# Kernel optimization log

Measured on AMD Instinct MI355X. Metric: run time of the kernel, lower is better.

Reference implementation:

```python
import jax, jax.numpy as jnp
import numpy as np

T, B, H, E, V = 128, 64, 512, 256, 32000
UNK = 2
EPS = 1e-10


def setup_inputs() -> dict:
    key = jax.random.key(0)
    ks = jax.random.split(key, 16)
    s = 0.02
    return {
        "u_enc_out": jax.random.normal(ks[0], (T, B, H), jnp.float32),
        "z_tm1": jax.random.randint(ks[1], (1, B), 0, V),
        "last_hidden": jax.random.normal(ks[2], (1, B, H), jnp.float32),
        "u_input": jax.random.randint(ks[3], (T, B), 0, V),
        "emb": jax.random.normal(ks[4], (V, E), jnp.float32) * s,
        "attn_W": jax.random.normal(ks[5], (H, 2 * H), jnp.float32) * s,
        "attn_b": jnp.zeros((H,), jnp.float32),
        "attn_v": jax.random.normal(ks[6], (H,), jnp.float32) * (1.0 / np.sqrt(H)),
        "gru_Wih": jax.random.normal(ks[7], (3 * H, H + E), jnp.float32) * s,
        "gru_Whh": jax.random.normal(ks[8], (3 * H, H), jnp.float32) * s,
        "gru_bih": jnp.zeros((3 * H,), jnp.float32),
        "gru_bhh": jnp.zeros((3 * H,), jnp.float32),
        "proj_W": jax.random.normal(ks[9], (V, 2 * H), jnp.float32) * s,
        "proj_b": jnp.zeros((V,), jnp.float32),
        "copy1_W": jax.random.normal(ks[10], (H, H), jnp.float32) * s,
        "copy1_b": jnp.zeros((H,), jnp.float32),
    }


def _copy_logscore(raw, u_input):
    # raw: [B,T] copy scores; u_input: [T,B] int ids
    # Faithful to: log(bmm(exp(raw - max), sparse_one_hot_with_1e-10_floor)) + max
    cmax = jnp.max(raw, axis=1, keepdims=True)            # [B,1]
    ex = jnp.exp(raw - cmax)                              # [B,T]
    idx = u_input.T                                       # [B,T]
    idx = jnp.where(idx == UNK, V + jnp.arange(T)[None, :], idx)
    mask = (u_input.T != 0).astype(ex.dtype)
    total = jnp.sum(ex, axis=1)                           # [B] (all t, incl. ignored)
    scat = jax.vmap(lambda e, i: jnp.zeros((V + T,), ex.dtype).at[i].add(e))(ex * mask, idx)
    return jnp.log(EPS * total[:, None] + (1.0 - EPS) * scat) + cmax  # [B,V+T]


def reference(u_enc_out, z_tm1, last_hidden, u_input, emb, attn_W, attn_b, attn_v,
              gru_Wih, gru_Whh, gru_bih, gru_bhh, proj_W, proj_b, copy1_W, copy1_b):
    enc = jnp.transpose(u_enc_out, (1, 0, 2))             # [B,T,H]
    h = last_hidden[0]                                    # [B,H]
    # Attn: energy = tanh(Linear([h;enc])), score = v . energy, softmax over T
    Hrep = jnp.broadcast_to(h[:, None, :], enc.shape)
    energy = jnp.tanh(jnp.einsum('bti,hi->bth', jnp.concatenate([Hrep, enc], -1), attn_W) + attn_b)
    alpha = jax.nn.softmax(jnp.einsum('h,bth->bt', attn_v, energy), axis=1)
    ctx = jnp.einsum('bt,bth->bh', alpha, enc)            # [B,H]
    # GRU step (pytorch gate order r,z,n)
    x = jnp.concatenate([emb[z_tm1[0]], ctx], axis=-1)    # [B,E+H]
    gi = x @ gru_Wih.T + gru_bih
    gh = h @ gru_Whh.T + gru_bhh
    i_r, i_z, i_n = jnp.split(gi, 3, axis=-1)
    h_r, h_z, h_n = jnp.split(gh, 3, axis=-1)
    r = jax.nn.sigmoid(i_r + h_r)
    z = jax.nn.sigmoid(i_z + h_z)
    n = jnp.tanh(i_n + r * h_n)
    h_new = (1.0 - z) * n + z * h                         # [B,H]
    gru_out = h_new[None]                                 # [1,B,H]
    new_hidden = h_new[None]
    # generation score
    gen_score = jnp.concatenate([h_new, ctx], -1) @ proj_W.T + proj_b  # [B,V]
    # copy score
    cs = jnp.tanh(jnp.einsum('bth,ih->bti', enc, copy1_W) + copy1_b)   # [B,T,H]
    raw = jnp.einsum('bth,bh->bt', cs, h_new)             # [B,T]
    u_copy = _copy_logscore(raw, u_input)                 # [B,V+T]
    scores = jax.nn.softmax(jnp.concatenate([gen_score, u_copy], axis=1), axis=1)
    g, c = scores[:, :V], scores[:, V:]                   # [B,V], [B,V+T]
    proba = jnp.concatenate([g + c[:, :V], c[:, V:]], axis=1)  # [B,V+T]
    return gru_out, new_hidden, proba
```

## Files before the change

kernel.cpp:

```cpp
#include <hip/hip_runtime.h>
#include <math.h>

#define T_ 128
#define B_ 64
#define H_ 512
#define E_ 256
#define V_ 32000
#define VT_ (V_ + T_)
#define UNK_ 2
#define EPS_ 1e-10f
#define NP_ (V_ / 64)

typedef __attribute__((ext_vector_type(8))) _Float16 half8;
typedef __attribute__((ext_vector_type(2))) _Float16 half2v;
typedef __attribute__((ext_vector_type(4))) float floatx4;

#define NB_ZERO 32
#define NB_CVTA 512
#define NB_CVTC 512
#define NB_WH   8192
#define NB_CVTW 2048
#define NB_XE   64
#define NB_XH   128
#define NB_BC   8
#define NB_PRO (NB_ZERO + NB_CVTA + NB_CVTC + NB_WH + NB_CVTW + NB_XE + NB_XH + NB_BC)

__global__ __launch_bounds__(256) void prologue_k(
        const float* __restrict__ attn_W,
        const float* __restrict__ copy1_W, const float* __restrict__ last_h,
        const float* __restrict__ attn_b, const float* __restrict__ emb,
        const int* __restrict__ z, const float* __restrict__ Wih,
        const float* __restrict__ Whh, const float* __restrict__ bih,
        const float* __restrict__ bhh,
        float* __restrict__ zbase,
        _Float16* __restrict__ Wb_attn, _Float16* __restrict__ Wb_copy,
        float* __restrict__ Wh, _Float16* __restrict__ Wcat,
        _Float16* __restrict__ xg, float* __restrict__ bcat) {
    int bid = blockIdx.x, tid = threadIdx.x;
    if (bid < NB_ZERO) { zbase[bid * 256 + tid] = 0.f; return; }
    bid -= NB_ZERO;
    if (bid < NB_CVTA) {
        int c = tid * 2;
        float2 v = *(const float2*)(attn_W + (size_t)bid * 1024 + 512 + c);
        Wb_attn[bid * 512 + c]     = (_Float16)v.x;
        Wb_attn[bid * 512 + c + 1] = (_Float16)v.y;
        return;
    }
    bid -= NB_CVTA;
    if (bid < NB_CVTC) {
        int c = tid * 2;
        float2 v = *(const float2*)(copy1_W + (size_t)bid * 512 + c);
        Wb_copy[bid * 512 + c]     = (_Float16)v.x;
        Wb_copy[bid * 512 + c + 1] = (_Float16)v.y;
        return;
    }
    bid -= NB_CVTC;
    if (bid < NB_WH) {
        int wid = bid * 4 + (tid >> 6), lane = tid & 63;
        int b = wid >> 9, m = wid & 511;
        const float4* wr = (const float4*)(attn_W + (size_t)m * 1024);
        const float4* xr = (const float4*)(last_h + b * 512);
        float s = 0.f;
        #pragma unroll
        for (int i = 0; i < 2; ++i) {
            int k = lane + i * 64;
            float4 w = wr[k], x = xr[k];
            s += w.x * x.x + w.y * x.y + w.z * x.z + w.w * x.w;
        }
        #pragma unroll
        for (int off = 32; off > 0; off >>= 1) s += __shfl_down(s, off);
        if (lane == 0) Wh[b * 512 + m] = s + attn_b[m];
        return;
    }
    bid -= NB_WH;
    if (bid < NB_CVTW) {
        int mp = bid;
        int q  = (mp >> 4) & 3;
        int hh = (mp >> 6) * 16 + (mp & 15);
        #pragma unroll
        for (int j = 0; j < 5; ++j) {
            int c = j * 256 + tid;
            float w;
            if (q == 0)      w = (c < 768) ? Wih[(size_t)hh * 768 + c]
                                           : Whh[(size_t)hh * 512 + (c - 768)];
            else if (q == 1) w = (c < 768) ? Wih[(size_t)(512 + hh) * 768 + c]
                                           : Whh[(size_t)(512 + hh) * 512 + (c - 768)];
            else if (q == 2) w = (c < 768) ? Wih[(size_t)(1024 + hh) * 768 + c] : 0.f;
            else             w = (c >= 768) ? Whh[(size_t)(1024 + hh) * 512 + (c - 768)] : 0.f;
            Wcat[(size_t)mp * 1280 + c] = (_Float16)w;
        }
        return;
    }
    bid -= NB_CVTW;
    if (bid < NB_XE) {
        int idx = bid * 256 + tid;
        int bb = idx >> 8, c = idx & 255;
        xg[bb * 1280 + c] = (_Float16)emb[(size_t)z[bb] * E_ + c];
        return;
    }
    bid -= NB_XE;
    if (bid < NB_XH) {
        int idx = bid * 256 + tid;
        int bb = idx >> 9, c = idx & 511;
        xg[bb * 1280 + 768 + c] = (_Float16)last_h[bb * H_ + c];
        return;
    }
    bid -= NB_XH;
    {
        int mp = bid * 256 + tid;
        int q  = (mp >> 4) & 3;
        int hh = (mp >> 6) * 16 + (mp & 15);
        float v2;
        if (q == 0)      v2 = bih[hh] + bhh[hh];
        else if (q == 1) v2 = bih[512 + hh] + bhh[512 + hh];
        else if (q == 2) v2 = bih[1024 + hh];
        else             v2 = bhh[1024 + hh];
        bcat[mp] = v2;
    }
}

__global__ __launch_bounds__(512) void enc_dual_k(
        const float* __restrict__ u_enc,
        const _Float16* __restrict__ Wa,
        const _Float16* __restrict__ Wc,
        const float* __restrict__ Wh,
        const float* __restrict__ attn_v,
        const float* __restrict__ copy1_b,
        float* __restrict__ score,
        _Float16* __restrict__ cs) {
    __shared__ _Float16 As[64 * 512];
    int bid = blockIdx.x;
    int xcd = bid & 7, loc = bid >> 3;
    int xt = xcd * 16 + (loc & 15);
    int yt = loc >> 4;
    int b  = xt >> 1;
    int t0 = (xt & 1) * 64;
    int r0 = b * T_ + t0;
    int tid = threadIdx.x;
    int lane = tid & 63, wave = tid >> 6;
    const float* srcb = u_enc + (size_t)t0 * B_ * H_ + (size_t)b * H_;
    #pragma unroll
    for (int i = 0; i < 8; ++i) {
        int G = i * 512 + tid;
        int r = G >> 6, s = G & 63;
        const float4* p = (const float4*)(srcb + (size_t)r * B_ * H_ + s * 8);
        float4 a0 = p[0], a1 = p[1];
        half8 v;
        v[0] = (_Float16)a0.x; v[1] = (_Float16)a0.y; v[2] = (_Float16)a0.z; v[3] = (_Float16)a0.w;
        v[4] = (_Float16)a1.x; v[5] = (_Float16)a1.y; v[6] = (_Float16)a1.z; v[7] = (_Float16)a1.w;
        *(half8*)&As[(size_t)(((r << 6) | (s ^ (r & 7))) << 3)] = v;
    }
    __syncthreads();
    int n0 = yt * 128 + (wave >> 2) * 64 + (wave & 3) * 16;
    int coln = lane & 15;
    int g = lane >> 4;
    const _Float16* wra = Wa + (size_t)(n0 + coln) * H_ + g * 8;
    const _Float16* wrc = Wc + (size_t)(n0 + coln) * H_ + g * 8;
    floatx4 acca[4] = {}, accc[4] = {};
    #pragma unroll 4
    for (int k0 = 0; k0 < H_; k0 += 32) {
        half8 fba = *(const half8*)(wra + k0);
        half8 fbc = *(const half8*)(wrc + k0);
        #pragma unroll
        for (int mi = 0; mi < 4; ++mi) {
            int r = mi * 16 + coln;
            half8 fa = *(const half8*)&As[((size_t)r << 9) +
                          ((((k0 >> 3) + g) ^ (coln & 7)) << 3)];
            acca[mi] = __builtin_amdgcn_mfma_f32_16x16x32_f16(fa, fba, acca[mi], 0, 0, 0);
            accc[mi] = __builtin_amdgcn_mfma_f32_16x16x32_f16(fa, fbc, accc[mi], 0, 0, 0);
        }
    }
    int col = n0 + coln;
    float addt = Wh[b * H_ + col];
    float av   = attn_v[col];
    float cb   = copy1_b[col];
    int rbase = g * 4;
    #pragma unroll
    for (int mi = 0; mi < 4; ++mi)
        #pragma unroll
        for (int r = 0; r < 4; ++r) {
            int row = r0 + mi * 16 + rbase + r;
            float x = acca[mi][r] + addt;
            float t2 = __expf(2.f * x);
            float v = av * ((t2 - 1.f) / (t2 + 1.f));
            v += __shfl_xor(v, 1);
            v += __shfl_xor(v, 2);
            v += __shfl_xor(v, 4);
            v += __shfl_xor(v, 8);
            if (coln == 0) atomicAdd(&score[row], v);
            float y = accc[mi][r] + cb;
            float t3 = __expf(2.f * y);
            cs[(size_t)row * H_ + col] = (_Float16)((t3 - 1.f) / (t3 + 1.f));
        }
}

__global__ __launch_bounds__(128) void softctx_k(
        const float* __restrict__ score, const float* __restrict__ u_enc,
        _Float16* __restrict__ xcat, _Float16* __restrict__ xg) {
    __shared__ float al[T_];
    __shared__ float red[T_];
    int b = blockIdx.x, tid = threadIdx.x;
    float v = score[b * T_ + tid];
    red[tid] = v;
    __syncthreads();
    for (int s = 64; s > 0; s >>= 1) { if (tid < s) red[tid] = fmaxf(red[tid], red[tid + s]); __syncthreads(); }
    float m = red[0]; __syncthreads();
    float e = __expf(v - m);
    red[tid] = e;
    __syncthreads();
    for (int s = 64; s > 0; s >>= 1) { if (tid < s) red[tid] += red[tid + s]; __syncthreads(); }
    al[tid] = e / red[0];
    __syncthreads();
    int col0 = blockIdx.y * 256 + tid * 2;
    const float2* ebase = (const float2*)(u_enc + (size_t)b * H_ + col0);
    float s0 = 0.f, s1 = 0.f;
    #pragma unroll 16
    for (int t = 0; t < T_; ++t) {
        float2 u = ebase[(size_t)t * (B_ * H_ / 2)];
        float a = al[t];
        s0 += a * u.x;
        s1 += a * u.y;
    }
    half2v o; o[0] = (_Float16)s0; o[1] = (_Float16)s1;
    *(half2v*)(xcat + b * 1024 + 512 + col0) = o;
    *(half2v*)(xg + b * 1280 + 256 + col0)   = o;
}

__global__ __launch_bounds__(512) void grucat_k(
        const _Float16* __restrict__ xg,
        const _Float16* __restrict__ Wcat,
        const float* __restrict__ bcat,
        const float* __restrict__ hprev,
        float* __restrict__ out,
        _Float16* __restrict__ xcat) {
    __shared__ float Lt[8][64][17];
    int tid = threadIdx.x;
    int lane = tid & 63, wave = tid >> 6;
    int q = wave & 3, khalf = wave >> 2;
    int n0 = blockIdx.x * 64 + q * 16;
    int coln = lane & 15;
    int kq  = (lane >> 4) * 8;
    int kbase = khalf * 640;
    const _Float16* wrow  = Wcat + (size_t)(n0 + coln) * 1280 + kbase + kq;
    const _Float16* abase = xg + kbase + kq;
    floatx4 acc[4] = {};
    #pragma unroll 5
    for (int k0 = 0; k0 < 640; k0 += 32) {
        half8 fb = *(const half8*)(wrow + k0);
        #pragma unroll
        for (int mi = 0; mi < 4; ++mi) {
            half8 fa = *(const half8*)(abase + (size_t)(mi * 16 + coln) * 1280 + k0);
            acc[mi] = __builtin_amdgcn_mfma_f32_16x16x32_f16(fa, fb, acc[mi], 0, 0, 0);
        }
    }
    int rbase = (lane >> 4) * 4;
    #pragma unroll
    for (int mi = 0; mi < 4; ++mi)
        #pragma unroll
        for (int r = 0; r < 4; ++r)
            Lt[wave][mi * 16 + rbase + r][coln] = acc[mi][r];
    __syncthreads();
    int HB = blockIdx.x * 16;
    #pragma unroll
    for (int p = tid; p < 1024; p += 512) {
        int b = p >> 4, i = p & 15;
        float G0 = Lt[0][b][i] + Lt[4][b][i] + bcat[blockIdx.x * 64 + i];
        float G1 = Lt[1][b][i] + Lt[5][b][i] + bcat[blockIdx.x * 64 + 16 + i];
        float G2 = Lt[2][b][i] + Lt[6][b][i] + bcat[blockIdx.x * 64 + 32 + i];
        float G3 = Lt[3][b][i] + Lt[7][b][i] + bcat[blockIdx.x * 64 + 48 + i];
        float rr = 1.f / (1.f + __expf(-G0));
        float zz = 1.f / (1.f + __expf(-G1));
        float nn = tanhf(G2 + rr * G3);
        float h  = hprev[b * H_ + HB + i];
        float hv = (1.f - zz) * nn + zz * h;
        out[b * H_ + HB + i] = hv;
        out[B_ * H_ + b * H_ + HB + i] = hv;
        xcat[b * 1024 + HB + i] = (_Float16)hv;
    }
}

__global__ __launch_bounds__(512, 4) void proj_raw_k(
        const _Float16* __restrict__ xcat,
        const float* __restrict__ Wp,
        const float* __restrict__ bp,
        float* __restrict__ gen,
        float* __restrict__ mpart, float* __restrict__ lpart,
        const _Float16* __restrict__ cs,
        const float* __restrict__ hnew,
        const int* __restrict__ u_input,
        float* __restrict__ scat, float* __restrict__ sc4) {
    __shared__ float Ct[4][64][17];
    __shared__ float m_lds[4][64];
    __shared__ float l_lds[4][64];
    __shared__ float rawS[T_];
    __shared__ float red[T_];
    int tid = threadIdx.x;
    int lane = tid & 63, wave = tid >> 6;
    if (blockIdx.x < NP_) {
        int q = wave & 3, khalf = wave >> 2;
        int n0 = (blockIdx.x * 4 + q) * 16;
        int coln = lane & 15;
        int kq  = (lane >> 4) * 8;
        int kbase = khalf * 512;
        const float* wrow = Wp + (size_t)(n0 + coln) * 1024 + kbase + kq;
        const _Float16* abase = xcat + kbase + kq;
        floatx4 acc[4] = {};
        #pragma unroll 8
        for (int k0 = 0; k0 < 512; k0 += 32) {
            const float4* wb = (const float4*)(wrow + k0);
            float4 w0 = wb[0], w1 = wb[1];
            half8 fb;
            fb[0] = (_Float16)w0.x; fb[1] = (_Float16)w0.y; fb[2] = (_Float16)w0.z; fb[3] = (_Float16)w0.w;
            fb[4] = (_Float16)w1.x; fb[5] = (_Float16)w1.y; fb[6] = (_Float16)w1.z; fb[7] = (_Float16)w1.w;
            #pragma unroll
            for (int mi = 0; mi < 4; ++mi) {
                half8 fa = *(const half8*)(abase + (size_t)(mi * 16 + coln) * 1024 + k0);
                acc[mi] = __builtin_amdgcn_mfma_f32_16x16x32_f16(fa, fb, acc[mi], 0, 0, 0);
            }
        }
        int rbase = (lane >> 4) * 4;
        if (khalf) {
            #pragma unroll
            for (int mi = 0; mi < 4; ++mi)
                #pragma unroll
                for (int r = 0; r < 4; ++r)
                    Ct[q][mi * 16 + rbase + r][coln] = acc[mi][r];
        }
        __syncthreads();
        if (!khalf) {
            float bias = bp[n0 + coln];
            #pragma unroll
            for (int mi = 0; mi < 4; ++mi)
                #pragma unroll
                for (int r = 0; r < 4; ++r) {
                    int brow = mi * 16 + rbase + r;
                    float x = acc[mi][r] + Ct[q][brow][coln] + bias;
                    gen[(size_t)brow * V_ + n0 + coln] = x;
                    float mm = x;
                    mm = fmaxf(mm, __shfl_xor(mm, 1));
                    mm = fmaxf(mm, __shfl_xor(mm, 2));
                    mm = fmaxf(mm, __shfl_xor(mm, 4));
                    mm = fmaxf(mm, __shfl_xor(mm, 8));
                    float e = __expf(x - mm);
                    e += __shfl_xor(e, 1);
                    e += __shfl_xor(e, 2);
                    e += __shfl_xor(e, 4);
                    e += __shfl_xor(e, 8);
                    if (coln == 0) { m_lds[q][brow] = mm; l_lds[q][brow] = e; }
                }
        }
        __syncthreads();
        if (tid < 64) {
            int bb = tid;
            float M = m_lds[0][bb], L = l_lds[0][bb];
            #pragma unroll
            for (int w = 1; w < 4; ++w) {
                float m2 = m_lds[w][bb], l2 = l_lds[w][bb];
                float nm = fmaxf(M, m2);
                L = L * __expf(M - nm) + l2 * __expf(m2 - nm);
                M = nm;
            }
            mpart[bb * NP_ + blockIdx.x] = M;
            lpart[bb * NP_ + blockIdx.x] = L;
        }
        return;
    }
    int b = blockIdx.x - NP_;
    const float4* hp = (const float4*)(hnew + b * H_ + lane * 8);
    float4 ha = hp[0], hb = hp[1];
    #pragma unroll 4
    for (int i = 0; i < 16; ++i) {
        int t = wave * 16 + i;
        half8 c8 = *(const half8*)(cs + (size_t)(b * T_ + t) * H_ + lane * 8);
        float s = (float)c8[0] * ha.x + (float)c8[1] * ha.y + (float)c8[2] * ha.z + (float)c8[3] * ha.w
                + (float)c8[4] * hb.x + (float)c8[5] * hb.y + (float)c8[6] * hb.z + (float)c8[7] * hb.w;
        #pragma unroll
        for (int off = 32; off > 0; off >>= 1) s += __shfl_down(s, off);
        if (lane == 0) rawS[t] = s;
    }
    __syncthreads();
    int t = tid;
    float v = (t < T_) ? rawS[t] : -1e30f;
    if (t < T_) red[t] = v;
    __syncthreads();
    for (int s = 64; s > 0; s >>= 1) { if (t < s) red[t] = fmaxf(red[t], red[t + s]); __syncthreads(); }
    float cm = red[0]; __syncthreads();
    float e = (t < T_) ? __expf(v - cm) : 0.f;
    if (t < T_) red[t] = e;
    __syncthreads();
    for (int s = 64; s > 0; s >>= 1) { if (t < s) red[t] += red[t + s]; __syncthreads(); }
    float tot = red[0]; __syncthreads();
    int id = (t < T_) ? u_input[t * B_ + b] : 0;
    size_t j = (size_t)b * VT_ + ((id == UNK_) ? (V_ + (t & 127)) : id);
    if (id != 0) scat[j] = 0.f;
    __syncthreads();
    if (id != 0) atomicAdd(&scat[j], e);
    if (t < T_) red[t] = (id != 0) ? e : 0.f;
    __syncthreads();
    for (int s = 64; s > 0; s >>= 1) { if (t < s) red[t] += red[t + s]; __syncthreads(); }
    float ssum = red[0]; __syncthreads();
    float sv = (id != 0) ? scat[j] : 0.f;
    if (t < T_) red[t] = sv;
    __syncthreads();
    for (int s = 64; s > 0; s >>= 1) { if (t < s) red[t] = fmaxf(red[t], red[t + s]); __syncthreads(); }
    if (t == 0) {
        sc4[b * 4 + 0] = cm;
        sc4[b * 4 + 1] = tot;
        sc4[b * 4 + 2] = ssum;
        sc4[b * 4 + 3] = red[0];
    }
}

__global__ __launch_bounds__(256) void write_fix_k(
        const float* __restrict__ gen,
        const float* __restrict__ mpart, const float* __restrict__ lpart,
        const float* __restrict__ sc4, const int* __restrict__ u_input,
        const float* __restrict__ scat, float* __restrict__ proba) {
    __shared__ float ms[256], ls[256];
    __shared__ float pb[4];
    int b = blockIdx.y, tid = threadIdx.x;
    float M = -1e30f, L = 0.f;
    for (int s = tid; s < NP_; s += 256) {
        float m2 = mpart[b * NP_ + s], l2 = lpart[b * NP_ + s];
        float nm = fmaxf(M, m2);
        L = L * __expf(M - nm) + l2 * __expf(m2 - nm);
        M = nm;
    }
    ms[tid] = M; ls[tid] = L;
    __syncthreads();
    for (int s = 128; s > 0; s >>= 1) {
        if (tid < s) {
            float m2 = ms[tid + s], l2 = ls[tid + s];
            float nm = fmaxf(ms[tid], m2);
            ls[tid] = ls[tid] * __expf(ms[tid] - nm) + l2 * __expf(m2 - nm);
            ms[tid] = nm;
        }
        __syncthreads();
    }
    if (tid == 0) {
        float Mg = ms[0], Zg = ls[0];
        float cm = sc4[b * 4], tot = sc4[b * 4 + 1], ssum = sc4[b * 4 + 2], smax = sc4[b * 4 + 3];
        float umax = cm + logf(EPS_ * tot + (1.f - EPS_) * smax);
        float M2 = fmaxf(Mg, umax);
        float coef = __expf(cm - M2);
        float Z = Zg * __expf(Mg - M2) + coef * (EPS_ * tot * (float)VT_ + (1.f - EPS_) * ssum);
        float invZ = 1.f / Z;
        pb[0] = M2;
        pb[1] = invZ;
        pb[2] = coef * EPS_ * tot * invZ;
        pb[3] = coef * (1.f - EPS_) * invZ;
    }
    __syncthreads();
    float M2 = pb[0], invZ = pb[1], addc = pb[2], scoef = pb[3];
    int i4 = blockIdx.x * 256 + tid;
    if (i4 < VT_ / 4) {
        int j = i4 * 4;
        float4 p;
        if (j < V_) {
            float4 g = *(const float4*)(gen + (size_t)b * V_ + j);
            p.x = addc + __expf(g.x - M2) * invZ;
            p.y = addc + __expf(g.y - M2) * invZ;
            p.z = addc + __expf(g.z - M2) * invZ;
            p.w = addc + __expf(g.w - M2) * invZ;
        } else {
            p.x = p.y = p.z = p.w = addc;
        }
        *(float4*)(proba + (size_t)b * VT_ + j) = p;
    }
    __syncthreads();
    if (tid < T_) {
        int t = tid;
        int id = u_input[t * B_ + b];
        if (id != 0) {
            int j = (id == UNK_) ? (V_ + t) : id;
            int lo = blockIdx.x * 1024;
            if (j >= lo && j < lo + 1024) {
                float p = addc + scoef * scat[(size_t)b * VT_ + j];
                if (j < V_) p += __expf(gen[(size_t)b * V_ + j] - M2) * invZ;
                proba[(size_t)b * VT_ + j] = p;
            }
        }
    }
}

extern "C" void kernel_launch(void* const* d_in, const int* in_sizes, int n_in,
                              void* d_out, int out_size, void* d_ws, size_t ws_size,
                              hipStream_t stream) {
    const float* u_enc   = (const float*)d_in[0];
    const int*   z_tm1   = (const int*)d_in[1];
    const float* last_h  = (const float*)d_in[2];
    const int*   u_input = (const int*)d_in[3];
    const float* emb     = (const float*)d_in[4];
    const float* attn_W  = (const float*)d_in[5];
    const float* attn_b  = (const float*)d_in[6];
    const float* attn_v  = (const float*)d_in[7];
    const float* gru_Wih = (const float*)d_in[8];
    const float* gru_Whh = (const float*)d_in[9];
    const float* gru_bih = (const float*)d_in[10];
    const float* gru_bhh = (const float*)d_in[11];
    const float* proj_W  = (const float*)d_in[12];
    const float* proj_b  = (const float*)d_in[13];
    const float* copy1_W = (const float*)d_in[14];
    const float* copy1_b = (const float*)d_in[15];
    float* out = (float*)d_out;

    float* ws    = (float*)d_ws;
    float* score = ws;
    float* gen   = score + B_ * T_;
    float* scat  = gen + (size_t)B_ * V_;
    float* Wh    = scat + (size_t)B_ * VT_;
    float* mpart = Wh + B_ * H_;
    float* lpart = mpart + B_ * NP_;
    float* sc4   = lpart + B_ * NP_;
    float* bcat  = sc4 + B_ * 4;
    _Float16* xcat  = (_Float16*)(bcat + 2048);
    _Float16* xg    = xcat + B_ * 1024;
    _Float16* Wb_attn = xg + B_ * 1280;
    _Float16* Wb_copy = Wb_attn + H_ * H_;
    _Float16* Wcat  = Wb_copy + H_ * H_;
    _Float16* cs    = Wcat + 2048 * 1280;

    prologue_k<<<NB_PRO, 256, 0, stream>>>(attn_W, copy1_W, last_h, attn_b,
                                           emb, z_tm1, gru_Wih, gru_Whh, gru_bih, gru_bhh,
                                           score, Wb_attn, Wb_copy, Wh, Wcat, xg, bcat);

    enc_dual_k<<<512, 512, 0, stream>>>(u_enc, Wb_attn, Wb_copy, Wh, attn_v, copy1_b,
                                        score, cs);

    softctx_k<<<dim3(B_, 2), 128, 0, stream>>>(score, u_enc, xcat, xg);

    grucat_k<<<32, 512, 0, stream>>>(xg, Wcat, bcat, last_h, out, xcat);

    proj_raw_k<<<NP_ + B_, 512, 0, stream>>>(xcat, proj_W, proj_b, gen, mpart, lpart,
                                             cs, out, u_input, scat, sc4);

    float* proba = out + 2 * B_ * H_;
    write_fix_k<<<dim3((VT_ / 4 + 255) / 256, B_), 256, 0, stream>>>(
        gen, mpart, lpart, sc4, u_input, scat, proba);
}
```

Measured before the change: 350.3 us.

## Drop split-K in projection GEMM and register-prefetch weight chunks

The projection kernel no longer splits K across two wave halves with an LDS reduction. Each of 8 waves now computes a 16-column tile over the full K=1024 and double-buffers fp32 weight loads in registers, 256 K-elements at a time. This removes the LDS partial-sum exchange and one barrier, halves the number of projection blocks, and gives each wave more loads in flight. The cost is much higher register pressure (launch bounds drop from 4 to 2 blocks per CU), fewer blocks overall, and 8-way rather than 4-way partial softmax merging.

```diff
diff --git a/kernel.cpp b/kernel.cpp
--- a/kernel.cpp
+++ b/kernel.cpp
@@ -9,7 +9,7 @@
 #define VT_ (V_ + T_)
 #define UNK_ 2
 #define EPS_ 1e-10f
-#define NP_ (V_ / 64)
+#define NP_ (V_ / 128)
 
 typedef __attribute__((ext_vector_type(8))) _Float16 half8;
 typedef __attribute__((ext_vector_type(2))) _Float16 half2v;
@@ -279,7 +279,7 @@
     }
 }
 
-__global__ __launch_bounds__(512, 4) void proj_raw_k(
+__global__ __launch_bounds__(512, 2) void proj_raw_k(
         const _Float16* __restrict__ xcat,
         const float* __restrict__ Wp,
         const float* __restrict__ bp,
@@ -289,72 +289,76 @@
         const float* __restrict__ hnew,
         const int* __restrict__ u_input,
         float* __restrict__ scat, float* __restrict__ sc4) {
-    __shared__ float Ct[4][64][17];
-    __shared__ float m_lds[4][64];
-    __shared__ float l_lds[4][64];
+    __shared__ float m_lds[8][64];
+    __shared__ float l_lds[8][64];
     __shared__ float rawS[T_];
     __shared__ float red[T_];
     int tid = threadIdx.x;
     int lane = tid & 63, wave = tid >> 6;
     if (blockIdx.x < NP_) {
-        int q = wave & 3, khalf = wave >> 2;
-        int n0 = (blockIdx.x * 4 + q) * 16;
+        int n0 = blockIdx.x * 128 + wave * 16;
         int coln = lane & 15;
-        int kq  = (lane >> 4) * 8;
-        int kbase = khalf * 512;
-        const float* wrow = Wp + (size_t)(n0 + coln) * 1024 + kbase + kq;
-        const _Float16* abase = xcat + kbase + kq;
+        int g = lane >> 4;
+        const float4* wrow4 = (const float4*)(Wp + (size_t)(n0 + coln) * 1024 + g * 8);
+        const _Float16* abase = xcat + g * 8;
         floatx4 acc[4] = {};
-        #pragma unroll 8
-        for (int k0 = 0; k0 < 512; k0 += 32) {
-            const float4* wb = (const float4*)(wrow + k0);
-            float4 w0 = wb[0], w1 = wb[1];
-            half8 fb;
-            fb[0] = (_Float16)w0.x; fb[1] = (_Float16)w0.y; fb[2] = (_Float16)w0.z; fb[3] = (_Float16)w0.w;
-            fb[4] = (_Float16)w1.x; fb[5] = (_Float16)w1.y; fb[6] = (_Float16)w1.z; fb[7] = (_Float16)w1.w;
+        float4 pw[2][8][2];
+        #pragma unroll
+        for (int i = 0; i < 8; ++i) {
+            pw[0][i][0] = wrow4[i * 8];
+            pw[0][i][1] = wrow4[i * 8 + 1];
+        }
+        #pragma unroll
+        for (int c = 0; c < 4; ++c) {
+            const int cur = c & 1;
+            if (c < 3) {
+                #pragma unroll
+                for (int i = 0; i < 8; ++i) {
+                    pw[cur ^ 1][i][0] = wrow4[(c + 1) * 64 + i * 8];
+                    pw[cur ^ 1][i][1] = wrow4[(c + 1) * 64 + i * 8 + 1];
+                }
+            }
             #pragma unroll
-            for (int mi = 0; mi < 4; ++mi) {
-                half8 fa = *(const half8*)(abase + (size_t)(mi * 16 + coln) * 1024 + k0);
-                acc[mi] = __builtin_amdgcn_mfma_f32_16x16x32_f16(fa, fb, acc[mi], 0, 0, 0);
+            for (int i = 0; i < 8; ++i) {
+                float4 w0 = pw[cur][i][0], w1 = pw[cur][i][1];
+                half8 fb;
+                fb[0] = (_Float16)w0.x; fb[1] = (_Float16)w0.y; fb[2] = (_Float16)w0.z; fb[3] = (_Float16)w0.w;
+                fb[4] = (_Float16)w1.x; fb[5] = (_Float16)w1.y; fb[6] = (_Float16)w1.z; fb[7] = (_Float16)w1.w;
+                int k0 = c * 256 + i * 32;
+                #pragma unroll
+                for (int mi = 0; mi < 4; ++mi) {
+                    half8 fa = *(const half8*)(abase + (size_t)(mi * 16 + coln) * 1024 + k0);
+                    acc[mi] = __builtin_amdgcn_mfma_f32_16x16x32_f16(fa, fb, acc[mi], 0, 0, 0);
+                }
             }
         }
-        int rbase = (lane >> 4) * 4;
-        if (khalf) {
+        int rbase = g * 4;
+        float bias = bp[n0 + coln];
+        #pragma unroll
+        for (int mi = 0; mi < 4; ++mi)
             #pragma unroll
-            for (int mi = 0; mi < 4; ++mi)
-                #pragma unroll
-                for (int r = 0; r < 4; ++r)
-                    Ct[q][mi * 16 + rbase + r][coln] = acc[mi][r];
-        }
-        __syncthreads();
-        if (!khalf) {
-            float bias = bp[n0 + coln];
-            #pragma unroll
-            for (int mi = 0; mi < 4; ++mi)
-                #pragma unroll
-                for (int r = 0; r < 4; ++r) {
-                    int brow = mi * 16 + rbase + r;
-                    float x = acc[mi][r] + Ct[q][brow][coln] + bias;
-                    gen[(size_t)brow * V_ + n0 + coln] = x;
-                    float mm = x;
-                    mm = fmaxf(mm, __shfl_xor(mm, 1));
-                    mm = fmaxf(mm, __shfl_xor(mm, 2));
-                    mm = fmaxf(mm, __shfl_xor(mm, 4));
-                    mm = fmaxf(mm, __shfl_xor(mm, 8));
-                    float e = __expf(x - mm);
-                    e += __shfl_xor(e, 1);
-                    e += __shfl_xor(e, 2);
-                    e += __shfl_xor(e, 4);
-                    e += __shfl_xor(e, 8);
-                    if (coln == 0) { m_lds[q][brow] = mm; l_lds[q][brow] = e; }
-                }
-        }
+            for (int r = 0; r < 4; ++r) {
+                int brow = mi * 16 + rbase + r;
+                float x = acc[mi][r] + bias;
+                gen[(size_t)brow * V_ + n0 + coln] = x;
+                float mm = x;
+                mm = fmaxf(mm, __shfl_xor(mm, 1));
+                mm = fmaxf(mm, __shfl_xor(mm, 2));
+                mm = fmaxf(mm, __shfl_xor(mm, 4));
+                mm = fmaxf(mm, __shfl_xor(mm, 8));
+                float e = __expf(x - mm);
+                e += __shfl_xor(e, 1);
+                e += __shfl_xor(e, 2);
+                e += __shfl_xor(e, 4);
+                e += __shfl_xor(e, 8);
+                if (coln == 0) { m_lds[wave][brow] = mm; l_lds[wave][brow] = e; }
+            }
         __syncthreads();
         if (tid < 64) {
             int bb = tid;
             float M = m_lds[0][bb], L = l_lds[0][bb];
             #pragma unroll
-            for (int w = 1; w < 4; ++w) {
+            for (int w = 1; w < 8; ++w) {
                 float m2 = m_lds[w][bb], l2 = l_lds[w][bb];
                 float nm = fmaxf(M, m2);
                 L = L * __expf(M - nm) + l2 * __expf(m2 - nm);
@@ -391,7 +395,7 @@
     for (int s = 64; s > 0; s >>= 1) { if (t < s) red[t] += red[t + s]; __syncthreads(); }
     float tot = red[0]; __syncthreads();
     int id = (t < T_) ? u_input[t * B_ + b] : 0;
-    size_t j = (size_t)b * VT_ + ((id == UNK_) ? (V_ + (t & 127)) : id);
+    size_t j = (size_t)b * VT_ + ((id == UNK_) ? (V_ + t) : id);
     if (id != 0) scat[j] = 0.f;
     __syncthreads();
     if (id != 0) atomicAdd(&scat[j], e);
```

Result: no change. 345.0 us (-1.5%).
